# Optimization experiments

Measured on AMD Instinct MI355X. Metric: run time of the kernel, lower is better.

Reference implementation:

```python
import jax, jax.numpy as jnp
import numpy as np

C = 256
DF = 8
CQK = C // DF  # 32


def setup_inputs() -> dict:
    key = jax.random.key(0)
    ks = jax.random.split(key, 7)
    s = 0.02
    x = jax.random.normal(ks[0], (4, C, 64, 64), dtype=jnp.float32)
    Wq = jax.random.normal(ks[1], (CQK, C), dtype=jnp.float32) * s
    bq = jnp.zeros((CQK,), dtype=jnp.float32)
    Wk = jax.random.normal(ks[2], (CQK, C), dtype=jnp.float32) * s
    bk = jnp.zeros((CQK,), dtype=jnp.float32)
    Wv = jax.random.normal(ks[3], (C, C), dtype=jnp.float32) * s
    bv = jnp.zeros((C,), dtype=jnp.float32)
    gamma = jnp.ones((1,), dtype=jnp.float32)  # nonzero so output is nontrivial
    return {"x": x, "Wq": Wq, "bq": bq, "Wk": Wk, "bk": bk, "Wv": Wv, "bv": bv, "gamma": gamma}


def reference(x, Wq, bq, Wk, bk, Wv, bv, gamma):
    B, Cc, H, W = x.shape
    # flatten spatial: [B, N, C] with N = H*W
    xf = x.reshape(B, Cc, H * W).transpose(0, 2, 1)
    # 1x1 convs == per-pixel linear projections
    q = jnp.einsum('bnc,dc->bnd', xf, Wq) + bq        # [B, N, Cqk]
    k = jnp.einsum('bnc,dc->bnd', xf, Wk) + bk        # [B, N, Cqk]
    v = jnp.einsum('bnc,dc->bnd', xf, Wv) + bv        # [B, N, C]
    energy = jnp.einsum('bnd,bmd->bnm', q, k)          # [B, N, N], no scale (as in source)
    attn = jax.nn.softmax(energy, axis=-1)
    out = jnp.einsum('bnm,bmc->bnc', attn, v)          # [B, N, C]
    out = out.transpose(0, 2, 1).reshape(B, Cc, H, W)
    return gamma[0] * out
```

## Files before the change

kernel.cpp:

```cpp
#include <hip/hip_runtime.h>
#include <hip/hip_bf16.h>


typedef __attribute__((ext_vector_type(8))) short s8v;
typedef __attribute__((ext_vector_type(4))) float f4v;

#define NPIX 4096
#define CIN 256
#define DQK 32

#if __has_builtin(__builtin_amdgcn_exp2f)
#define EXP2(x) __builtin_amdgcn_exp2f(x)
#else
#define EXP2(x) exp2f(x)
#endif

#if __has_builtin(__builtin_amdgcn_s_waitcnt)
#define LGKM0_BARRIER() { __builtin_amdgcn_s_waitcnt(0xC07F); __builtin_amdgcn_s_barrier(); }
#else
#define LGKM0_BARRIER() { __asm__ __volatile__("s_waitcnt lgkmcnt(0)\n\ts_barrier" ::: "memory"); }
#endif

static __device__ __forceinline__ unsigned short f2bf(float f) {
    union { float f; unsigned int u; } v; v.f = f;
    unsigned int r = v.u + 0x7FFF + ((v.u >> 16) & 1);
    return (unsigned short)(r >> 16);
}
static __device__ __forceinline__ unsigned int fbits(float f) {
    union { float f; unsigned int u; } v; v.f = f; return v.u;
}

__global__ void wcast_kernel(const float* __restrict__ Wq, const float* __restrict__ bq,
                             const float* __restrict__ Wk, const float* __restrict__ bk,
                             const float* __restrict__ Wv, const float* __restrict__ bv,
                             unsigned short* __restrict__ Wall, float* __restrict__ ball) {
    int row = blockIdx.x;
    int t = threadIdx.x;
    const float* src; const float* bsrc;
    if (row < 32)       { src = Wq + row * 256;        bsrc = bq + row; }
    else if (row < 64)  { src = Wk + (row - 32) * 256; bsrc = bk + (row - 32); }
    else                { src = Wv + (row - 64) * 256; bsrc = bv + (row - 64); }
    Wall[row * 256 + t] = f2bf(src[t]);
    if (t == 0) ball[row] = bsrc[0];
}

__global__ void tcast_kernel(const float* __restrict__ x, unsigned short* __restrict__ xT) {
    __shared__ unsigned short tile[64][65];
    int bidx = blockIdx.x;
    int b    = bidx >> 8;
    int cblk = (bidx >> 6) & 3;
    int nblk = bidx & 63;
    int t = threadIdx.x;
    int c0 = cblk * 64, n0 = nblk * 64;
    const float* xb = x + (size_t)b * CIN * NPIX;
    #pragma unroll
    for (int p = 0; p < 4; p++) {
        int cl = p * 16 + (t >> 4);
        int nl = (t & 15) * 4;
        float4 v = *(const float4*)(xb + (size_t)(c0 + cl) * NPIX + n0 + nl);
        tile[cl][nl + 0] = f2bf(v.x);
        tile[cl][nl + 1] = f2bf(v.y);
        tile[cl][nl + 2] = f2bf(v.z);
        tile[cl][nl + 3] = f2bf(v.w);
    }
    __syncthreads();
    unsigned short* xTb = xT + (size_t)b * NPIX * CIN;
    #pragma unroll
    for (int p = 0; p < 4; p++) {
        int nl = p * 16 + (t >> 4);
        int cl = (t & 15) * 4;
        ushort4 wv;
        wv.x = tile[cl + 0][nl];
        wv.y = tile[cl + 1][nl];
        wv.z = tile[cl + 2][nl];
        wv.w = tile[cl + 3][nl];
        *(ushort4*)(xTb + (size_t)(n0 + nl) * CIN + c0 + cl) = wv;
    }
}

__global__ __launch_bounds__(256)
void proj_kernel(const unsigned short* __restrict__ xT,
                 const unsigned short* __restrict__ Wall,
                 const float* __restrict__ ball,
                 unsigned short* __restrict__ Q,
                 unsigned short* __restrict__ Kp,
                 unsigned short* __restrict__ Vt) {
    int idx  = blockIdx.x;
    int b    = (idx & 7) >> 1;
    int nblk = ((idx >> 3) << 1) | (idx & 1);
    int w    = threadIdx.x >> 6;
    int lane = threadIdx.x & 63;
    int l16 = lane & 15, quad = lane >> 4;
    int n0 = nblk * 64 + w * 16;

    const unsigned short* brow = xT + (size_t)(b * NPIX + n0 + l16) * CIN + quad * 8;
    s8v bfr[8];
    #pragma unroll
    for (int kk = 0; kk < 8; kk++) bfr[kk] = *(const s8v*)(brow + kk * 32);

    #pragma unroll
    for (int p = 0; p < 10; p++) {
        const unsigned short* w0 = Wall + (size_t)(2 * p * 16 + l16) * CIN + quad * 8;
        const unsigned short* w1 = w0 + 16 * CIN;
        f4v a0 = {0.f, 0.f, 0.f, 0.f}, a1 = {0.f, 0.f, 0.f, 0.f};
        if (p < 2) {
            #pragma unroll
            for (int kk = 0; kk < 8; kk++) {
                a0 = __builtin_amdgcn_mfma_f32_16x16x32_bf16(bfr[kk], *(const s8v*)(w0 + kk * 32), a0, 0, 0, 0);
                a1 = __builtin_amdgcn_mfma_f32_16x16x32_bf16(bfr[kk], *(const s8v*)(w1 + kk * 32), a1, 0, 0, 0);
            }
        } else {
            #pragma unroll
            for (int kk = 0; kk < 8; kk++) {
                a0 = __builtin_amdgcn_mfma_f32_16x16x32_bf16(*(const s8v*)(w0 + kk * 32), bfr[kk], a0, 0, 0, 0);
                a1 = __builtin_amdgcn_mfma_f32_16x16x32_bf16(*(const s8v*)(w1 + kk * 32), bfr[kk], a1, 0, 0, 0);
            }
        }
        #pragma unroll
        for (int half = 0; half < 2; half++) {
            int ob = 2 * p + half;
            f4v acc = half ? a1 : a0;
            if (ob < 2) {
                int oc = ob * 16 + l16;
                float bias = ball[oc];
                #pragma unroll
                for (int r = 0; r < 4; r++) {
                    int n = n0 + quad * 4 + r;
                    Q[(size_t)(b * NPIX + n) * DQK + oc] =
                        f2bf((acc[r] + bias) * 1.44269504f);
                }
            } else if (ob < 4) {
                int oc = (ob - 2) * 16 + l16;
                float bias = ball[32 + oc];
                #pragma unroll
                for (int r = 0; r < 4; r++) {
                    int n = n0 + quad * 4 + r;
                    int pn = (n & ~31) | (((n >> 2) & 1) << 4) | (((n >> 3) & 3) << 2) | (n & 3);
                    Kp[(size_t)(b * NPIX + pn) * DQK + oc] = f2bf(acc[r] + bias);
                }
            } else {
                int n = n0 + l16;
                #pragma unroll
                for (int r = 0; r < 4; r++) {
                    int ch = (ob - 4) * 16 + quad * 4 + r;
                    Vt[((size_t)b * CIN + ch) * NPIX + n] = f2bf(acc[r] + ball[64 + ch]);
                }
            }
        }
    }
}

#define ATTN_STEP(S, WB, KC0, KC1, VC, KN0, KN1, VN)                            \
    {                                                                           \
        const int kvn = ((S) + 1) & 63;                                         \
        KN0 = *(const s8v*)(kbase + (size_t)(kvn * 64) * DQK);                  \
        KN1 = *(const s8v*)(kbase + (size_t)(kvn * 64 + 16) * DQK);             \
        _Pragma("unroll")                                                       \
        for (int ct = 0; ct < 4; ct++)                                          \
            VN[ct] = *(const s8v*)(vbase + (size_t)ct * 16 * NPIX + (S) * 64);  \
        const unsigned int* rb = smemw + khw + (1 - (WB)) * 1024;               \
        s8v pa0 = (cj == 0) ? ppv : *(const s8v*)(rb + rdo0);                   \
        s8v pa1 = (cj == 1) ? ppv : *(const s8v*)(rb + rdo1);                   \
        s8v pa2 = (cj == 2) ? ppv : *(const s8v*)(rb + rdo2);                   \
        s8v pa3 = (cj == 3) ? ppv : *(const s8v*)(rb + rdo3);                   \
        f4v s0 = {0.f, 0.f, 0.f, 0.f}, s1 = {0.f, 0.f, 0.f, 0.f};               \
        s0 = __builtin_amdgcn_mfma_f32_16x16x32_bf16(KC0, qf, s0, 0, 0, 0);     \
        s1 = __builtin_amdgcn_mfma_f32_16x16x32_bf16(KC1, qf, s1, 0, 0, 0);     \
        float p00 = EXP2(s0[0]), p01 = EXP2(s0[1]);                             \
        float p02 = EXP2(s0[2]), p03 = EXP2(s0[3]);                             \
        float p10 = EXP2(s1[0]), p11 = EXP2(s1[1]);                             \
        float p12 = EXP2(s1[2]), p13 = EXP2(s1[3]);                             \
        lsum += ((p00 + p01) + (p02 + p03)) + ((p10 + p11) + (p12 + p13));      \
        union { uint4 u; s8v v; } pp;                                           \
        pp.u.x = __builtin_amdgcn_perm(fbits(p01), fbits(p00), 0x07060302);     \
        pp.u.y = __builtin_amdgcn_perm(fbits(p03), fbits(p02), 0x07060302);     \
        pp.u.z = __builtin_amdgcn_perm(fbits(p11), fbits(p10), 0x07060302);     \
        pp.u.w = __builtin_amdgcn_perm(fbits(p13), fbits(p12), 0x07060302);     \
        *(uint4*)(smemw + khw + (WB) * 1024 + wro) = pp.u;                      \
        _Pragma("unroll")                                                       \
        for (int ct = 0; ct < 4; ct++) {                                        \
            O[0][ct] = __builtin_amdgcn_mfma_f32_16x16x32_bf16(VC[ct], pa0, O[0][ct], 0, 0, 0); \
            O[1][ct] = __builtin_amdgcn_mfma_f32_16x16x32_bf16(VC[ct], pa1, O[1][ct], 0, 0, 0); \
            O[2][ct] = __builtin_amdgcn_mfma_f32_16x16x32_bf16(VC[ct], pa2, O[2][ct], 0, 0, 0); \
            O[3][ct] = __builtin_amdgcn_mfma_f32_16x16x32_bf16(VC[ct], pa3, O[3][ct], 0, 0, 0); \
        }                                                                       \
        LGKM0_BARRIER();                                                        \
        ppv = pp.v;                                                             \
    }

__global__ __launch_bounds__(512)
void attn_kernel(const unsigned short* __restrict__ Q,
                 const unsigned short* __restrict__ Kp,
                 const unsigned short* __restrict__ Vt,
                 const float* __restrict__ gamma,
                 float* __restrict__ out) {
    __shared__ __align__(16) char smem[70144];
    unsigned int* smemw = (unsigned int*)smem;

    int idx = blockIdx.x;
    int b      = (idx & 7) >> 1;
    int rowblk = ((idx >> 3) << 1) | (idx & 1);

    int lane = threadIdx.x & 63;
    int w    = threadIdx.x >> 6;
    int l16 = lane & 15, quad = lane >> 4;
    int kh = w >> 2;
    int cj = w & 3;

    const unsigned short* Kb = Kp + (size_t)b * NPIX * DQK;
    const unsigned short* Vb = Vt + (size_t)b * CIN * NPIX;

    int rowbase = rowblk * 64;
    const s8v qf = *(const s8v*)(Q + (size_t)(b * NPIX + rowbase + cj * 16 + l16) * DQK + quad * 8);

    const unsigned short* kbase = Kb + (32 * kh + l16) * DQK + quad * 8;
    const unsigned short* vbase = Vb + (size_t)(cj * 64 + l16) * NPIX + 32 * kh + quad * 8;

    const int khw  = kh * 2048;
    const int wro  = l16 * 64 + (((cj * 4 + quad) ^ (l16 & 7)) << 2);
    const int rdo0 = l16 * 64 + (((0 * 4 + quad) ^ (l16 & 7)) << 2);
    const int rdo1 = l16 * 64 + (((1 * 4 + quad) ^ (l16 & 7)) << 2);
    const int rdo2 = l16 * 64 + (((2 * 4 + quad) ^ (l16 & 7)) << 2);
    const int rdo3 = l16 * 64 + (((3 * 4 + quad) ^ (l16 & 7)) << 2);

    f4v O[4][4];
    #pragma unroll
    for (int rt = 0; rt < 4; rt++)
        #pragma unroll
        for (int ct = 0; ct < 4; ct++) O[rt][ct] = (f4v){0.f, 0.f, 0.f, 0.f};
    float lsum = 0.f;
    s8v ppv;

    s8v Kc0, Kc1, Kn0, Kn1, Vc[4], Vn[4];
    Kc0 = *(const s8v*)(kbase);
    Kc1 = *(const s8v*)(kbase + 16 * DQK);

    {
        Kn0 = *(const s8v*)(kbase + (size_t)64 * DQK);
        Kn1 = *(const s8v*)(kbase + (size_t)80 * DQK);
        #pragma unroll
        for (int ct = 0; ct < 4; ct++)
            Vc[ct] = *(const s8v*)(vbase + (size_t)ct * 16 * NPIX);
        f4v s0 = {0.f, 0.f, 0.f, 0.f}, s1 = {0.f, 0.f, 0.f, 0.f};
        s0 = __builtin_amdgcn_mfma_f32_16x16x32_bf16(Kc0, qf, s0, 0, 0, 0);
        s1 = __builtin_amdgcn_mfma_f32_16x16x32_bf16(Kc1, qf, s1, 0, 0, 0);
        float p00 = EXP2(s0[0]), p01 = EXP2(s0[1]);
        float p02 = EXP2(s0[2]), p03 = EXP2(s0[3]);
        float p10 = EXP2(s1[0]), p11 = EXP2(s1[1]);
        float p12 = EXP2(s1[2]), p13 = EXP2(s1[3]);
        lsum += ((p00 + p01) + (p02 + p03)) + ((p10 + p11) + (p12 + p13));
        union { uint4 u; s8v v; } pp;
        pp.u.x = __builtin_amdgcn_perm(fbits(p01), fbits(p00), 0x07060302);
        pp.u.y = __builtin_amdgcn_perm(fbits(p03), fbits(p02), 0x07060302);
        pp.u.z = __builtin_amdgcn_perm(fbits(p11), fbits(p10), 0x07060302);
        pp.u.w = __builtin_amdgcn_perm(fbits(p13), fbits(p12), 0x07060302);
        *(uint4*)(smemw + khw + 0 * 1024 + wro) = pp.u;
        LGKM0_BARRIER();
        ppv = pp.v;
    }

    for (int p = 0; p < 31; p++) {
        int s1i = 2 * p + 1;
        ATTN_STEP(s1i,     1, Kn0, Kn1, Vc, Kc0, Kc1, Vn);
        ATTN_STEP(s1i + 1, 0, Kc0, Kc1, Vn, Kn0, Kn1, Vc);
    }
    ATTN_STEP(63, 1, Kn0, Kn1, Vc, Kc0, Kc1, Vn);

    {
        const unsigned int* rb = smemw + khw + 1024;
        s8v pa0 = (cj == 0) ? ppv : *(const s8v*)(rb + rdo0);
        s8v pa1 = (cj == 1) ? ppv : *(const s8v*)(rb + rdo1);
        s8v pa2 = (cj == 2) ? ppv : *(const s8v*)(rb + rdo2);
        s8v pa3 = (cj == 3) ? ppv : *(const s8v*)(rb + rdo3);
        #pragma unroll
        for (int ct = 0; ct < 4; ct++) {
            O[0][ct] = __builtin_amdgcn_mfma_f32_16x16x32_bf16(Vn[ct], pa0, O[0][ct], 0, 0, 0);
            O[1][ct] = __builtin_amdgcn_mfma_f32_16x16x32_bf16(Vn[ct], pa1, O[1][ct], 0, 0, 0);
            O[2][ct] = __builtin_amdgcn_mfma_f32_16x16x32_bf16(Vn[ct], pa2, O[2][ct], 0, 0, 0);
            O[3][ct] = __builtin_amdgcn_mfma_f32_16x16x32_bf16(Vn[ct], pa3, O[3][ct], 0, 0, 0);
        }
    }

    lsum += __shfl_xor(lsum, 16);
    lsum += __shfl_xor(lsum, 32);

    __syncthreads();

    float (*ldsO)[64][68] = (float (*)[64][68])smem;
    float* ldsL = (float*)(smem + 69632);

    if (quad == 0) ldsL[kh * 64 + cj * 16 + l16] = lsum;
    if (kh == 1) {
        #pragma unroll
        for (int rt = 0; rt < 4; rt++)
            #pragma unroll
            for (int ct = 0; ct < 4; ct++)
                *(f4v*)&ldsO[cj][lane][(rt * 4 + ct) * 4] = O[rt][ct];
    }
    __syncthreads();

    if (kh == 0) {
        float g = gamma[0];
        float rinv[4];
        #pragma unroll
        for (int rt = 0; rt < 4; rt++)
            rinv[rt] = g / (ldsL[rt * 16 + l16] + ldsL[64 + rt * 16 + l16]);
        #pragma unroll
        for (int rt = 0; rt < 4; rt++) {
            #pragma unroll
            for (int ct = 0; ct < 4; ct++) {
                f4v o2 = *(const f4v*)&ldsO[cj][lane][(rt * 4 + ct) * 4];
                #pragma unroll
                for (int r = 0; r < 4; r++) {
                    int ch = cj * 64 + ct * 16 + quad * 4 + r;
                    out[((size_t)b * CIN + ch) * NPIX + rowbase + rt * 16 + l16] =
                        (O[rt][ct][r] + o2[r]) * rinv[rt];
                }
            }
        }
    }
}

extern "C" void kernel_launch(void* const* d_in, const int* in_sizes, int n_in,
                              void* d_out, int out_size, void* d_ws, size_t ws_size,
                              hipStream_t stream) {
    const float* x     = (const float*)d_in[0];
    const float* Wq    = (const float*)d_in[1];
    const float* bq    = (const float*)d_in[2];
    const float* Wk    = (const float*)d_in[3];
    const float* bk    = (const float*)d_in[4];
    const float* Wv    = (const float*)d_in[5];
    const float* bv    = (const float*)d_in[6];
    const float* gamma = (const float*)d_in[7];
    float* out = (float*)d_out;

    char* p = (char*)d_ws;
    unsigned short* xT   = (unsigned short*)p; p += (size_t)4 * NPIX * CIN * 2;
    unsigned short* Qb   = (unsigned short*)p; p += (size_t)4 * NPIX * DQK * 2;
    unsigned short* Kb   = (unsigned short*)p; p += (size_t)4 * NPIX * DQK * 2;
    unsigned short* Vt   = (unsigned short*)p; p += (size_t)4 * CIN * NPIX * 2;
    unsigned short* Wall = (unsigned short*)p; p += (size_t)320 * 256 * 2;
    float*          ball = (float*)p;          p += (size_t)320 * 4;

    wcast_kernel<<<320, 256, 0, stream>>>(Wq, bq, Wk, bk, Wv, bv, Wall, ball);
    tcast_kernel<<<1024, 256, 0, stream>>>(x, xT);
    proj_kernel<<<256, 256, 0, stream>>>(xT, Wall, ball, Qb, Kb, Vt);
    attn_kernel<<<256, 512, 0, stream>>>(Qb, Kb, Vt, gamma, out);
}
```

Before: 183.4 us.

## Batch four attention steps per LDS barrier with deeper P buffering

Restructures the attention main loop so each wave computes four consecutive QK/softmax sub-steps, writing P tiles into four LDS slots per buffer set, before one barrier. Previously there was a barrier after every step. The change cuts barrier count by four and lets the PV MFMAs of one interval overlap the QK work of the next. In exchange it quadruples per-kh LDS usage for P (khw stride from 2048 to 8192 words), holds four P fragments in registers, and lengthens the V-load pipeline lag, which raises register pressure.

```diff
diff --git a/kernel.cpp b/kernel.cpp
--- a/kernel.cpp
+++ b/kernel.cpp
@@ -150,19 +150,25 @@
     }
 }
 
-#define ATTN_STEP(S, WB, KC0, KC1, VC, KN0, KN1, VN)                            \
+#define SUB_STEP(TB, J, SETW, DOPV, DOVL, KC0, KC1, KN0, KN1, VC, VN, PPV)      \
     {                                                                           \
-        const int kvn = ((S) + 1) & 63;                                         \
+        const int t_ = (TB) + (J);                                              \
+        const int kvn = (t_ + 1) & 63;                                          \
         KN0 = *(const s8v*)(kbase + (size_t)(kvn * 64) * DQK);                  \
         KN1 = *(const s8v*)(kbase + (size_t)(kvn * 64 + 16) * DQK);             \
-        _Pragma("unroll")                                                       \
-        for (int ct = 0; ct < 4; ct++)                                          \
-            VN[ct] = *(const s8v*)(vbase + (size_t)ct * 16 * NPIX + (S) * 64);  \
-        const unsigned int* rb = smemw + khw + (1 - (WB)) * 1024;               \
-        s8v pa0 = (cj == 0) ? ppv : *(const s8v*)(rb + rdo0);                   \
-        s8v pa1 = (cj == 1) ? ppv : *(const s8v*)(rb + rdo1);                   \
-        s8v pa2 = (cj == 2) ? ppv : *(const s8v*)(rb + rdo2);                   \
-        s8v pa3 = (cj == 3) ? ppv : *(const s8v*)(rb + rdo3);                   \
+        if (DOVL) {                                                             \
+            _Pragma("unroll")                                                   \
+            for (int ct = 0; ct < 4; ct++)                                      \
+                VN[ct] = *(const s8v*)(vbase + (size_t)ct * 16 * NPIX + (t_ - 3) * 64); \
+        }                                                                       \
+        s8v pa0, pa1, pa2, pa3;                                                 \
+        if (DOPV) {                                                             \
+            const unsigned int* rb = smemw + khw + ((1 - (SETW)) * 4 + (J)) * 1024; \
+            pa0 = (cj == 0) ? PPV : *(const s8v*)(rb + rdo0);                   \
+            pa1 = (cj == 1) ? PPV : *(const s8v*)(rb + rdo1);                   \
+            pa2 = (cj == 2) ? PPV : *(const s8v*)(rb + rdo2);                   \
+            pa3 = (cj == 3) ? PPV : *(const s8v*)(rb + rdo3);                   \
+        }                                                                       \
         f4v s0 = {0.f, 0.f, 0.f, 0.f}, s1 = {0.f, 0.f, 0.f, 0.f};               \
         s0 = __builtin_amdgcn_mfma_f32_16x16x32_bf16(KC0, qf, s0, 0, 0, 0);     \
         s1 = __builtin_amdgcn_mfma_f32_16x16x32_bf16(KC1, qf, s1, 0, 0, 0);     \
@@ -176,7 +182,38 @@
         pp.u.y = __builtin_amdgcn_perm(fbits(p03), fbits(p02), 0x07060302);     \
         pp.u.z = __builtin_amdgcn_perm(fbits(p11), fbits(p10), 0x07060302);     \
         pp.u.w = __builtin_amdgcn_perm(fbits(p13), fbits(p12), 0x07060302);     \
-        *(uint4*)(smemw + khw + (WB) * 1024 + wro) = pp.u;                      \
+        *(uint4*)(smemw + khw + ((SETW) * 4 + (J)) * 1024 + wro) = pp.u;        \
+        if (DOPV) {                                                             \
+            _Pragma("unroll")                                                   \
+            for (int ct = 0; ct < 4; ct++) {                                    \
+                O[0][ct] = __builtin_amdgcn_mfma_f32_16x16x32_bf16(VC[ct], pa0, O[0][ct], 0, 0, 0); \
+                O[1][ct] = __builtin_amdgcn_mfma_f32_16x16x32_bf16(VC[ct], pa1, O[1][ct], 0, 0, 0); \
+                O[2][ct] = __builtin_amdgcn_mfma_f32_16x16x32_bf16(VC[ct], pa2, O[2][ct], 0, 0, 0); \
+                O[3][ct] = __builtin_amdgcn_mfma_f32_16x16x32_bf16(VC[ct], pa3, O[3][ct], 0, 0, 0); \
+            }                                                                   \
+        }                                                                       \
+        PPV = pp.v;                                                             \
+    }
+
+#define INTERVAL4(TB, SETW)                                                     \
+    SUB_STEP(TB, 0, SETW, 1, 1, Kc0, Kc1, Kn0, Kn1, Vc, Vn, ppv0)               \
+    SUB_STEP(TB, 1, SETW, 1, 1, Kn0, Kn1, Kc0, Kc1, Vn, Vc, ppv1)               \
+    SUB_STEP(TB, 2, SETW, 1, 1, Kc0, Kc1, Kn0, Kn1, Vc, Vn, ppv2)               \
+    SUB_STEP(TB, 3, SETW, 1, 1, Kn0, Kn1, Kc0, Kc1, Vn, Vc, ppv3)               \
+    LGKM0_BARRIER();
+
+#define EPI_STEP(J, VC, VN, PPV, DOVL)                                          \
+    {                                                                           \
+        if (DOVL) {                                                             \
+            _Pragma("unroll")                                                   \
+            for (int ct = 0; ct < 4; ct++)                                      \
+                VN[ct] = *(const s8v*)(vbase + (size_t)ct * 16 * NPIX + (61 + (J)) * 64); \
+        }                                                                       \
+        const unsigned int* rb = smemw + khw + (4 + (J)) * 1024;                \
+        s8v pa0 = (cj == 0) ? PPV : *(const s8v*)(rb + rdo0);                   \
+        s8v pa1 = (cj == 1) ? PPV : *(const s8v*)(rb + rdo1);                   \
+        s8v pa2 = (cj == 2) ? PPV : *(const s8v*)(rb + rdo2);                   \
+        s8v pa3 = (cj == 3) ? PPV : *(const s8v*)(rb + rdo3);                   \
         _Pragma("unroll")                                                       \
         for (int ct = 0; ct < 4; ct++) {                                        \
             O[0][ct] = __builtin_amdgcn_mfma_f32_16x16x32_bf16(VC[ct], pa0, O[0][ct], 0, 0, 0); \
@@ -184,8 +221,6 @@
             O[2][ct] = __builtin_amdgcn_mfma_f32_16x16x32_bf16(VC[ct], pa2, O[2][ct], 0, 0, 0); \
             O[3][ct] = __builtin_amdgcn_mfma_f32_16x16x32_bf16(VC[ct], pa3, O[3][ct], 0, 0, 0); \
         }                                                                       \
-        LGKM0_BARRIER();                                                        \
-        ppv = pp.v;                                                             \
     }
 
 __global__ __launch_bounds__(512)
@@ -216,7 +251,7 @@
     const unsigned short* kbase = Kb + (32 * kh + l16) * DQK + quad * 8;
     const unsigned short* vbase = Vb + (size_t)(cj * 64 + l16) * NPIX + 32 * kh + quad * 8;
 
-    const int khw  = kh * 2048;
+    const int khw  = kh * 8192;
     const int wro  = l16 * 64 + (((cj * 4 + quad) ^ (l16 & 7)) << 2);
     const int rdo0 = l16 * 64 + (((0 * 4 + quad) ^ (l16 & 7)) << 2);
     const int rdo1 = l16 * 64 + (((1 * 4 + quad) ^ (l16 & 7)) << 2);
@@ -229,57 +264,30 @@
         #pragma unroll
         for (int ct = 0; ct < 4; ct++) O[rt][ct] = (f4v){0.f, 0.f, 0.f, 0.f};
     float lsum = 0.f;
-    s8v ppv;
+    s8v ppv0, ppv1, ppv2, ppv3;
 
     s8v Kc0, Kc1, Kn0, Kn1, Vc[4], Vn[4];
     Kc0 = *(const s8v*)(kbase);
     Kc1 = *(const s8v*)(kbase + 16 * DQK);
 
-    {
-        Kn0 = *(const s8v*)(kbase + (size_t)64 * DQK);
-        Kn1 = *(const s8v*)(kbase + (size_t)80 * DQK);
-        #pragma unroll
-        for (int ct = 0; ct < 4; ct++)
-            Vc[ct] = *(const s8v*)(vbase + (size_t)ct * 16 * NPIX);
-        f4v s0 = {0.f, 0.f, 0.f, 0.f}, s1 = {0.f, 0.f, 0.f, 0.f};
-        s0 = __builtin_amdgcn_mfma_f32_16x16x32_bf16(Kc0, qf, s0, 0, 0, 0);
-        s1 = __builtin_amdgcn_mfma_f32_16x16x32_bf16(Kc1, qf, s1, 0, 0, 0);
-        float p00 = EXP2(s0[0]), p01 = EXP2(s0[1]);
-        float p02 = EXP2(s0[2]), p03 = EXP2(s0[3]);
-        float p10 = EXP2(s1[0]), p11 = EXP2(s1[1]);
-        float p12 = EXP2(s1[2]), p13 = EXP2(s1[3]);
-        lsum += ((p00 + p01) + (p02 + p03)) + ((p10 + p11) + (p12 + p13));
-        union { uint4 u; s8v v; } pp;
-        pp.u.x = __builtin_amdgcn_perm(fbits(p01), fbits(p00), 0x07060302);
-        pp.u.y = __builtin_amdgcn_perm(fbits(p03), fbits(p02), 0x07060302);
-        pp.u.z = __builtin_amdgcn_perm(fbits(p11), fbits(p10), 0x07060302);
-        pp.u.w = __builtin_amdgcn_perm(fbits(p13), fbits(p12), 0x07060302);
-        *(uint4*)(smemw + khw + 0 * 1024 + wro) = pp.u;
-        LGKM0_BARRIER();
-        ppv = pp.v;
-    }
-
-    for (int p = 0; p < 31; p++) {
-        int s1i = 2 * p + 1;
-        ATTN_STEP(s1i,     1, Kn0, Kn1, Vc, Kc0, Kc1, Vn);
-        ATTN_STEP(s1i + 1, 0, Kc0, Kc1, Vn, Kn0, Kn1, Vc);
-    }
-    ATTN_STEP(63, 1, Kn0, Kn1, Vc, Kc0, Kc1, Vn);
-
-    {
-        const unsigned int* rb = smemw + khw + 1024;
-        s8v pa0 = (cj == 0) ? ppv : *(const s8v*)(rb + rdo0);
-        s8v pa1 = (cj == 1) ? ppv : *(const s8v*)(rb + rdo1);
-        s8v pa2 = (cj == 2) ? ppv : *(const s8v*)(rb + rdo2);
-        s8v pa3 = (cj == 3) ? ppv : *(const s8v*)(rb + rdo3);
-        #pragma unroll
-        for (int ct = 0; ct < 4; ct++) {
-            O[0][ct] = __builtin_amdgcn_mfma_f32_16x16x32_bf16(Vn[ct], pa0, O[0][ct], 0, 0, 0);
-            O[1][ct] = __builtin_amdgcn_mfma_f32_16x16x32_bf16(Vn[ct], pa1, O[1][ct], 0, 0, 0);
-            O[2][ct] = __builtin_amdgcn_mfma_f32_16x16x32_bf16(Vn[ct], pa2, O[2][ct], 0, 0, 0);
-            O[3][ct] = __builtin_amdgcn_mfma_f32_16x16x32_bf16(Vn[ct], pa3, O[3][ct], 0, 0, 0);
-        }
-    }
+    SUB_STEP(0, 0, 0, 0, 0, Kc0, Kc1, Kn0, Kn1, Vc, Vn, ppv0)
+    SUB_STEP(0, 1, 0, 0, 0, Kn0, Kn1, Kc0, Kc1, Vn, Vc, ppv1)
+    SUB_STEP(0, 2, 0, 0, 0, Kc0, Kc1, Kn0, Kn1, Vc, Vn, ppv2)
+    SUB_STEP(0, 3, 0, 0, 1, Kn0, Kn1, Kc0, Kc1, Vn, Vc, ppv3)
+    LGKM0_BARRIER();
+
+    int tb = 4;
+    for (int p = 0; p < 7; p++) {
+        INTERVAL4(tb, 1)
+        INTERVAL4(tb + 4, 0)
+        tb += 8;
+    }
+    INTERVAL4(60, 1)
+
+    EPI_STEP(0, Vc, Vn, ppv0, 1)
+    EPI_STEP(1, Vn, Vc, ppv1, 1)
+    EPI_STEP(2, Vc, Vn, ppv2, 1)
+    EPI_STEP(3, Vn, Vc, ppv3, 0)
 
     lsum += __shfl_xor(lsum, 16);
     lsum += __shfl_xor(lsum, 32);
```

After: 184.5 us. No clear change (+0.6%).

## Split attention key range across two wave groups with 1024-thread blocks

Applied to the files above, without the earlier changes.

Doubles the attention block to 1024 threads. The key/value sequence is split into two halves handled by separate 8-wave groups, each running 32 steps instead of 64, and the partial outputs and row sums are combined through LDS at the end. The aim is to shorten each block's serial loop and raise the number of waves per CU, since only 256 blocks run on a device with 256 CUs. In exchange it uses about 140KB of dynamic LDS, adds extra reduction barriers, and may raise register pressure under the 1024-thread launch bound. It also relies on dynamic shared memory above the default limit.

```diff
diff --git a/kernel.cpp b/kernel.cpp
--- a/kernel.cpp
+++ b/kernel.cpp
@@ -8,6 +8,7 @@
 #define NPIX 4096
 #define CIN 256
 #define DQK 32
+#define ATTN_LDS 140288
 
 #if __has_builtin(__builtin_amdgcn_exp2f)
 #define EXP2(x) __builtin_amdgcn_exp2f(x)
@@ -152,13 +153,13 @@
 
 #define ATTN_STEP(S, WB, KC0, KC1, VC, KN0, KN1, VN)                            \
     {                                                                           \
-        const int kvn = ((S) + 1) & 63;                                         \
+        const int kvn = ((S) + 1) & 31;                                         \
         KN0 = *(const s8v*)(kbase + (size_t)(kvn * 64) * DQK);                  \
         KN1 = *(const s8v*)(kbase + (size_t)(kvn * 64 + 16) * DQK);             \
         _Pragma("unroll")                                                       \
         for (int ct = 0; ct < 4; ct++)                                          \
             VN[ct] = *(const s8v*)(vbase + (size_t)ct * 16 * NPIX + (S) * 64);  \
-        const unsigned int* rb = smemw + khw + (1 - (WB)) * 1024;               \
+        const unsigned int* rb = smemw + gw + (1 - (WB)) * 1024;                \
         s8v pa0 = (cj == 0) ? ppv : *(const s8v*)(rb + rdo0);                   \
         s8v pa1 = (cj == 1) ? ppv : *(const s8v*)(rb + rdo1);                   \
         s8v pa2 = (cj == 2) ? ppv : *(const s8v*)(rb + rdo2);                   \
@@ -176,7 +177,7 @@
         pp.u.y = __builtin_amdgcn_perm(fbits(p03), fbits(p02), 0x07060302);     \
         pp.u.z = __builtin_amdgcn_perm(fbits(p11), fbits(p10), 0x07060302);     \
         pp.u.w = __builtin_amdgcn_perm(fbits(p13), fbits(p12), 0x07060302);     \
-        *(uint4*)(smemw + khw + (WB) * 1024 + wro) = pp.u;                      \
+        *(uint4*)(smemw + gw + (WB) * 1024 + wro) = pp.u;                       \
         _Pragma("unroll")                                                       \
         for (int ct = 0; ct < 4; ct++) {                                        \
             O[0][ct] = __builtin_amdgcn_mfma_f32_16x16x32_bf16(VC[ct], pa0, O[0][ct], 0, 0, 0); \
@@ -188,13 +189,13 @@
         ppv = pp.v;                                                             \
     }
 
-__global__ __launch_bounds__(512)
+__global__ __launch_bounds__(1024)
 void attn_kernel(const unsigned short* __restrict__ Q,
                  const unsigned short* __restrict__ Kp,
                  const unsigned short* __restrict__ Vt,
                  const float* __restrict__ gamma,
                  float* __restrict__ out) {
-    __shared__ __align__(16) char smem[70144];
+    extern __shared__ __align__(16) char smem[];
     unsigned int* smemw = (unsigned int*)smem;
 
     int idx = blockIdx.x;
@@ -204,8 +205,10 @@
     int lane = threadIdx.x & 63;
     int w    = threadIdx.x >> 6;
     int l16 = lane & 15, quad = lane >> 4;
-    int kh = w >> 2;
-    int cj = w & 3;
+    int khalf = w >> 3;
+    int kh    = (w >> 2) & 1;
+    int cj    = w & 3;
+    int grp   = khalf * 2 + kh;
 
     const unsigned short* Kb = Kp + (size_t)b * NPIX * DQK;
     const unsigned short* Vb = Vt + (size_t)b * CIN * NPIX;
@@ -213,10 +216,10 @@
     int rowbase = rowblk * 64;
     const s8v qf = *(const s8v*)(Q + (size_t)(b * NPIX + rowbase + cj * 16 + l16) * DQK + quad * 8);
 
-    const unsigned short* kbase = Kb + (32 * kh + l16) * DQK + quad * 8;
-    const unsigned short* vbase = Vb + (size_t)(cj * 64 + l16) * NPIX + 32 * kh + quad * 8;
-
-    const int khw  = kh * 2048;
+    const unsigned short* kbase = Kb + (size_t)(khalf * 2048 + 32 * kh + l16) * DQK + quad * 8;
+    const unsigned short* vbase = Vb + (size_t)(cj * 64 + l16) * NPIX + khalf * 2048 + 32 * kh + quad * 8;
+
+    const int gw   = grp * 2048;
     const int wro  = l16 * 64 + (((cj * 4 + quad) ^ (l16 & 7)) << 2);
     const int rdo0 = l16 * 64 + (((0 * 4 + quad) ^ (l16 & 7)) << 2);
     const int rdo1 = l16 * 64 + (((1 * 4 + quad) ^ (l16 & 7)) << 2);
@@ -254,20 +257,20 @@
         pp.u.y = __builtin_amdgcn_perm(fbits(p03), fbits(p02), 0x07060302);
         pp.u.z = __builtin_amdgcn_perm(fbits(p11), fbits(p10), 0x07060302);
         pp.u.w = __builtin_amdgcn_perm(fbits(p13), fbits(p12), 0x07060302);
-        *(uint4*)(smemw + khw + 0 * 1024 + wro) = pp.u;
+        *(uint4*)(smemw + gw + 0 * 1024 + wro) = pp.u;
         LGKM0_BARRIER();
         ppv = pp.v;
     }
 
-    for (int p = 0; p < 31; p++) {
+    for (int p = 0; p < 15; p++) {
         int s1i = 2 * p + 1;
         ATTN_STEP(s1i,     1, Kn0, Kn1, Vc, Kc0, Kc1, Vn);
         ATTN_STEP(s1i + 1, 0, Kc0, Kc1, Vn, Kn0, Kn1, Vc);
     }
-    ATTN_STEP(63, 1, Kn0, Kn1, Vc, Kc0, Kc1, Vn);
+    ATTN_STEP(31, 1, Kn0, Kn1, Vc, Kc0, Kc1, Vn);
 
     {
-        const unsigned int* rb = smemw + khw + 1024;
+        const unsigned int* rb = smemw + gw + 1024;
         s8v pa0 = (cj == 0) ? ppv : *(const s8v*)(rb + rdo0);
         s8v pa1 = (cj == 1) ? ppv : *(const s8v*)(rb + rdo1);
         s8v pa2 = (cj == 2) ? ppv : *(const s8v*)(rb + rdo2);
@@ -286,30 +289,52 @@
 
     __syncthreads();
 
-    float (*ldsO)[64][68] = (float (*)[64][68])smem;
-    float* ldsL = (float*)(smem + 69632);
-
-    if (quad == 0) ldsL[kh * 64 + cj * 16 + l16] = lsum;
+    float (*ldsO)[4][64][68] = (float (*)[4][64][68])smem;
+    float* ldsL = (float*)(smem + 139264);
+
+    if (quad == 0) ldsL[grp * 64 + cj * 16 + l16] = lsum;
     if (kh == 1) {
         #pragma unroll
         for (int rt = 0; rt < 4; rt++)
             #pragma unroll
             for (int ct = 0; ct < 4; ct++)
-                *(f4v*)&ldsO[cj][lane][(rt * 4 + ct) * 4] = O[rt][ct];
+                *(f4v*)&ldsO[khalf][cj][lane][(rt * 4 + ct) * 4] = O[rt][ct];
     }
     __syncthreads();
 
     if (kh == 0) {
+        #pragma unroll
+        for (int rt = 0; rt < 4; rt++)
+            #pragma unroll
+            for (int ct = 0; ct < 4; ct++) {
+                f4v o2 = *(const f4v*)&ldsO[khalf][cj][lane][(rt * 4 + ct) * 4];
+                O[rt][ct][0] += o2[0]; O[rt][ct][1] += o2[1];
+                O[rt][ct][2] += o2[2]; O[rt][ct][3] += o2[3];
+            }
+    }
+    __syncthreads();
+
+    if (kh == 0 && khalf == 1) {
+        #pragma unroll
+        for (int rt = 0; rt < 4; rt++)
+            #pragma unroll
+            for (int ct = 0; ct < 4; ct++)
+                *(f4v*)&ldsO[1][cj][lane][(rt * 4 + ct) * 4] = O[rt][ct];
+    }
+    __syncthreads();
+
+    if (kh == 0 && khalf == 0) {
         float g = gamma[0];
         float rinv[4];
         #pragma unroll
         for (int rt = 0; rt < 4; rt++)
-            rinv[rt] = g / (ldsL[rt * 16 + l16] + ldsL[64 + rt * 16 + l16]);
+            rinv[rt] = g / (ldsL[rt * 16 + l16] + ldsL[64 + rt * 16 + l16] +
+                            ldsL[128 + rt * 16 + l16] + ldsL[192 + rt * 16 + l16]);
         #pragma unroll
         for (int rt = 0; rt < 4; rt++) {
             #pragma unroll
             for (int ct = 0; ct < 4; ct++) {
-                f4v o2 = *(const f4v*)&ldsO[cj][lane][(rt * 4 + ct) * 4];
+                f4v o2 = *(const f4v*)&ldsO[1][cj][lane][(rt * 4 + ct) * 4];
                 #pragma unroll
                 for (int r = 0; r < 4; r++) {
                     int ch = cj * 64 + ct * 16 + quad * 4 + r;
@@ -345,5 +370,5 @@
     wcast_kernel<<<320, 256, 0, stream>>>(Wq, bq, Wk, bk, Wv, bv, Wall, ball);
     tcast_kernel<<<1024, 256, 0, stream>>>(x, xT);
     proj_kernel<<<256, 256, 0, stream>>>(xT, Wall, ball, Qb, Kb, Vt);
-    attn_kernel<<<256, 512, 0, stream>>>(Qb, Kb, Vt, gamma, out);
-}
+    attn_kernel<<<256, 1024, ATTN_LDS, stream>>>(Qb, Kb, Vt, gamma, out);
+}
```

Result: slower. 296.2 us (+61.5%).

## Halve attention row tile to 32 rows and double grid to 512 blocks

Applied to the files above, without the earlier changes.

Each attention block now handles 32 query rows instead of 64, and the grid doubles to 512 blocks. Only the two waves per key-half whose column group matches (isS) compute the QK scores and exp, sharing P through half-size LDS buffers. Each wave keeps half the output accumulators, which should lower register and LDS pressure and fill more CUs on a 256-CU part. In exchange, every K/V tile is streamed twice as many times overall, and the other waves sit idle during the score phase.

```diff
diff --git a/kernel.cpp b/kernel.cpp
--- a/kernel.cpp
+++ b/kernel.cpp
@@ -153,39 +153,39 @@
 #define ATTN_STEP(S, WB, KC0, KC1, VC, KN0, KN1, VN)                            \
     {                                                                           \
         const int kvn = ((S) + 1) & 63;                                         \
-        KN0 = *(const s8v*)(kbase + (size_t)(kvn * 64) * DQK);                  \
-        KN1 = *(const s8v*)(kbase + (size_t)(kvn * 64 + 16) * DQK);             \
+        if (isS) {                                                              \
+            KN0 = *(const s8v*)(kbase + (size_t)(kvn * 64) * DQK);              \
+            KN1 = *(const s8v*)(kbase + (size_t)(kvn * 64 + 16) * DQK);         \
+        }                                                                       \
         _Pragma("unroll")                                                       \
         for (int ct = 0; ct < 4; ct++)                                          \
             VN[ct] = *(const s8v*)(vbase + (size_t)ct * 16 * NPIX + (S) * 64);  \
-        const unsigned int* rb = smemw + khw + (1 - (WB)) * 1024;               \
-        s8v pa0 = (cj == 0) ? ppv : *(const s8v*)(rb + rdo0);                   \
-        s8v pa1 = (cj == 1) ? ppv : *(const s8v*)(rb + rdo1);                   \
-        s8v pa2 = (cj == 2) ? ppv : *(const s8v*)(rb + rdo2);                   \
-        s8v pa3 = (cj == 3) ? ppv : *(const s8v*)(rb + rdo3);                   \
-        f4v s0 = {0.f, 0.f, 0.f, 0.f}, s1 = {0.f, 0.f, 0.f, 0.f};               \
-        s0 = __builtin_amdgcn_mfma_f32_16x16x32_bf16(KC0, qf, s0, 0, 0, 0);     \
-        s1 = __builtin_amdgcn_mfma_f32_16x16x32_bf16(KC1, qf, s1, 0, 0, 0);     \
-        float p00 = EXP2(s0[0]), p01 = EXP2(s0[1]);                             \
-        float p02 = EXP2(s0[2]), p03 = EXP2(s0[3]);                             \
-        float p10 = EXP2(s1[0]), p11 = EXP2(s1[1]);                             \
-        float p12 = EXP2(s1[2]), p13 = EXP2(s1[3]);                             \
-        lsum += ((p00 + p01) + (p02 + p03)) + ((p10 + p11) + (p12 + p13));      \
+        const unsigned int* rb = smemw + khw + (1 - (WB)) * 512;                \
+        s8v pa0 = (isS && srt == 0) ? ppv : *(const s8v*)(rb + rdo0);           \
+        s8v pa1 = (isS && srt == 1) ? ppv : *(const s8v*)(rb + rdo1);           \
         union { uint4 u; s8v v; } pp;                                           \
-        pp.u.x = __builtin_amdgcn_perm(fbits(p01), fbits(p00), 0x07060302);     \
-        pp.u.y = __builtin_amdgcn_perm(fbits(p03), fbits(p02), 0x07060302);     \
-        pp.u.z = __builtin_amdgcn_perm(fbits(p11), fbits(p10), 0x07060302);     \
-        pp.u.w = __builtin_amdgcn_perm(fbits(p13), fbits(p12), 0x07060302);     \
-        *(uint4*)(smemw + khw + (WB) * 1024 + wro) = pp.u;                      \
+        if (isS) {                                                              \
+            f4v s0 = {0.f, 0.f, 0.f, 0.f}, s1 = {0.f, 0.f, 0.f, 0.f};           \
+            s0 = __builtin_amdgcn_mfma_f32_16x16x32_bf16(KC0, qf, s0, 0, 0, 0); \
+            s1 = __builtin_amdgcn_mfma_f32_16x16x32_bf16(KC1, qf, s1, 0, 0, 0); \
+            float p00 = EXP2(s0[0]), p01 = EXP2(s0[1]);                         \
+            float p02 = EXP2(s0[2]), p03 = EXP2(s0[3]);                         \
+            float p10 = EXP2(s1[0]), p11 = EXP2(s1[1]);                         \
+            float p12 = EXP2(s1[2]), p13 = EXP2(s1[3]);                         \
+            lsum += ((p00 + p01) + (p02 + p03)) + ((p10 + p11) + (p12 + p13));  \
+            pp.u.x = __builtin_amdgcn_perm(fbits(p01), fbits(p00), 0x07060302); \
+            pp.u.y = __builtin_amdgcn_perm(fbits(p03), fbits(p02), 0x07060302); \
+            pp.u.z = __builtin_amdgcn_perm(fbits(p11), fbits(p10), 0x07060302); \
+            pp.u.w = __builtin_amdgcn_perm(fbits(p13), fbits(p12), 0x07060302); \
+            *(uint4*)(smemw + khw + (WB) * 512 + wro) = pp.u;                   \
+        }                                                                       \
         _Pragma("unroll")                                                       \
         for (int ct = 0; ct < 4; ct++) {                                        \
             O[0][ct] = __builtin_amdgcn_mfma_f32_16x16x32_bf16(VC[ct], pa0, O[0][ct], 0, 0, 0); \
             O[1][ct] = __builtin_amdgcn_mfma_f32_16x16x32_bf16(VC[ct], pa1, O[1][ct], 0, 0, 0); \
-            O[2][ct] = __builtin_amdgcn_mfma_f32_16x16x32_bf16(VC[ct], pa2, O[2][ct], 0, 0, 0); \
-            O[3][ct] = __builtin_amdgcn_mfma_f32_16x16x32_bf16(VC[ct], pa3, O[3][ct], 0, 0, 0); \
         }                                                                       \
         LGKM0_BARRIER();                                                        \
-        ppv = pp.v;                                                             \
+        if (isS) ppv = pp.v;                                                    \
     }
 
 __global__ __launch_bounds__(512)
@@ -194,7 +194,7 @@
                  const unsigned short* __restrict__ Vt,
                  const float* __restrict__ gamma,
                  float* __restrict__ out) {
-    __shared__ __align__(16) char smem[70144];
+    __shared__ __align__(16) char smem[37120];
     unsigned int* smemw = (unsigned int*)smem;
 
     int idx = blockIdx.x;
@@ -206,57 +206,63 @@
     int l16 = lane & 15, quad = lane >> 4;
     int kh = w >> 2;
     int cj = w & 3;
+    int srt = cj & 1;
+    int isS = ((cj >> 1) == kh);
 
     const unsigned short* Kb = Kp + (size_t)b * NPIX * DQK;
     const unsigned short* Vb = Vt + (size_t)b * CIN * NPIX;
 
-    int rowbase = rowblk * 64;
-    const s8v qf = *(const s8v*)(Q + (size_t)(b * NPIX + rowbase + cj * 16 + l16) * DQK + quad * 8);
+    int rowbase = rowblk * 32;
+    const s8v qf = *(const s8v*)(Q + (size_t)(b * NPIX + rowbase + srt * 16 + l16) * DQK + quad * 8);
 
     const unsigned short* kbase = Kb + (32 * kh + l16) * DQK + quad * 8;
     const unsigned short* vbase = Vb + (size_t)(cj * 64 + l16) * NPIX + 32 * kh + quad * 8;
 
-    const int khw  = kh * 2048;
-    const int wro  = l16 * 64 + (((cj * 4 + quad) ^ (l16 & 7)) << 2);
-    const int rdo0 = l16 * 64 + (((0 * 4 + quad) ^ (l16 & 7)) << 2);
-    const int rdo1 = l16 * 64 + (((1 * 4 + quad) ^ (l16 & 7)) << 2);
-    const int rdo2 = l16 * 64 + (((2 * 4 + quad) ^ (l16 & 7)) << 2);
-    const int rdo3 = l16 * 64 + (((3 * 4 + quad) ^ (l16 & 7)) << 2);
-
-    f4v O[4][4];
-    #pragma unroll
-    for (int rt = 0; rt < 4; rt++)
+    const int khw  = kh * 1024;
+    const int wro  = l16 * 32 + (((srt * 4 + quad) ^ (l16 & 7)) << 2);
+    const int rdo0 = l16 * 32 + (((0 * 4 + quad) ^ (l16 & 7)) << 2);
+    const int rdo1 = l16 * 32 + (((1 * 4 + quad) ^ (l16 & 7)) << 2);
+
+    f4v O[2][4];
+    #pragma unroll
+    for (int rt = 0; rt < 2; rt++)
         #pragma unroll
         for (int ct = 0; ct < 4; ct++) O[rt][ct] = (f4v){0.f, 0.f, 0.f, 0.f};
     float lsum = 0.f;
     s8v ppv;
 
     s8v Kc0, Kc1, Kn0, Kn1, Vc[4], Vn[4];
-    Kc0 = *(const s8v*)(kbase);
-    Kc1 = *(const s8v*)(kbase + 16 * DQK);
+    if (isS) {
+        Kc0 = *(const s8v*)(kbase);
+        Kc1 = *(const s8v*)(kbase + 16 * DQK);
+    }
 
     {
-        Kn0 = *(const s8v*)(kbase + (size_t)64 * DQK);
-        Kn1 = *(const s8v*)(kbase + (size_t)80 * DQK);
+        if (isS) {
+            Kn0 = *(const s8v*)(kbase + (size_t)64 * DQK);
+            Kn1 = *(const s8v*)(kbase + (size_t)80 * DQK);
+        }
         #pragma unroll
         for (int ct = 0; ct < 4; ct++)
             Vc[ct] = *(const s8v*)(vbase + (size_t)ct * 16 * NPIX);
-        f4v s0 = {0.f, 0.f, 0.f, 0.f}, s1 = {0.f, 0.f, 0.f, 0.f};
-        s0 = __builtin_amdgcn_mfma_f32_16x16x32_bf16(Kc0, qf, s0, 0, 0, 0);
-        s1 = __builtin_amdgcn_mfma_f32_16x16x32_bf16(Kc1, qf, s1, 0, 0, 0);
-        float p00 = EXP2(s0[0]), p01 = EXP2(s0[1]);
-        float p02 = EXP2(s0[2]), p03 = EXP2(s0[3]);
-        float p10 = EXP2(s1[0]), p11 = EXP2(s1[1]);
-        float p12 = EXP2(s1[2]), p13 = EXP2(s1[3]);
-        lsum += ((p00 + p01) + (p02 + p03)) + ((p10 + p11) + (p12 + p13));
-        union { uint4 u; s8v v; } pp;
-        pp.u.x = __builtin_amdgcn_perm(fbits(p01), fbits(p00), 0x07060302);
-        pp.u.y = __builtin_amdgcn_perm(fbits(p03), fbits(p02), 0x07060302);
-        pp.u.z = __builtin_amdgcn_perm(fbits(p11), fbits(p10), 0x07060302);
-        pp.u.w = __builtin_amdgcn_perm(fbits(p13), fbits(p12), 0x07060302);
-        *(uint4*)(smemw + khw + 0 * 1024 + wro) = pp.u;
+        if (isS) {
+            f4v s0 = {0.f, 0.f, 0.f, 0.f}, s1 = {0.f, 0.f, 0.f, 0.f};
+            s0 = __builtin_amdgcn_mfma_f32_16x16x32_bf16(Kc0, qf, s0, 0, 0, 0);
+            s1 = __builtin_amdgcn_mfma_f32_16x16x32_bf16(Kc1, qf, s1, 0, 0, 0);
+            float p00 = EXP2(s0[0]), p01 = EXP2(s0[1]);
+            float p02 = EXP2(s0[2]), p03 = EXP2(s0[3]);
+            float p10 = EXP2(s1[0]), p11 = EXP2(s1[1]);
+            float p12 = EXP2(s1[2]), p13 = EXP2(s1[3]);
+            lsum += ((p00 + p01) + (p02 + p03)) + ((p10 + p11) + (p12 + p13));
+            union { uint4 u; s8v v; } pp;
+            pp.u.x = __builtin_amdgcn_perm(fbits(p01), fbits(p00), 0x07060302);
+            pp.u.y = __builtin_amdgcn_perm(fbits(p03), fbits(p02), 0x07060302);
+            pp.u.z = __builtin_amdgcn_perm(fbits(p11), fbits(p10), 0x07060302);
+            pp.u.w = __builtin_amdgcn_perm(fbits(p13), fbits(p12), 0x07060302);
+            *(uint4*)(smemw + khw + 0 * 512 + wro) = pp.u;
+            ppv = pp.v;
+        }
         LGKM0_BARRIER();
-        ppv = pp.v;
     }
 
     for (int p = 0; p < 31; p++) {
@@ -267,17 +273,13 @@
     ATTN_STEP(63, 1, Kn0, Kn1, Vc, Kc0, Kc1, Vn);
 
     {
-        const unsigned int* rb = smemw + khw + 1024;
-        s8v pa0 = (cj == 0) ? ppv : *(const s8v*)(rb + rdo0);
-        s8v pa1 = (cj == 1) ? ppv : *(const s8v*)(rb + rdo1);
-        s8v pa2 = (cj == 2) ? ppv : *(const s8v*)(rb + rdo2);
-        s8v pa3 = (cj == 3) ? ppv : *(const s8v*)(rb + rdo3);
+        const unsigned int* rb = smemw + khw + 512;
+        s8v pa0 = (isS && srt == 0) ? ppv : *(const s8v*)(rb + rdo0);
+        s8v pa1 = (isS && srt == 1) ? ppv : *(const s8v*)(rb + rdo1);
         #pragma unroll
         for (int ct = 0; ct < 4; ct++) {
             O[0][ct] = __builtin_amdgcn_mfma_f32_16x16x32_bf16(Vn[ct], pa0, O[0][ct], 0, 0, 0);
             O[1][ct] = __builtin_amdgcn_mfma_f32_16x16x32_bf16(Vn[ct], pa1, O[1][ct], 0, 0, 0);
-            O[2][ct] = __builtin_amdgcn_mfma_f32_16x16x32_bf16(Vn[ct], pa2, O[2][ct], 0, 0, 0);
-            O[3][ct] = __builtin_amdgcn_mfma_f32_16x16x32_bf16(Vn[ct], pa3, O[3][ct], 0, 0, 0);
         }
     }
 
@@ -286,13 +288,13 @@
 
     __syncthreads();
 
-    float (*ldsO)[64][68] = (float (*)[64][68])smem;
-    float* ldsL = (float*)(smem + 69632);
-
-    if (quad == 0) ldsL[kh * 64 + cj * 16 + l16] = lsum;
+    float (*ldsO)[64][36] = (float (*)[64][36])smem;
+    float* ldsL = (float*)(smem + 36864);
+
+    if (isS && quad == 0) ldsL[kh * 32 + srt * 16 + l16] = lsum;
     if (kh == 1) {
         #pragma unroll
-        for (int rt = 0; rt < 4; rt++)
+        for (int rt = 0; rt < 2; rt++)
             #pragma unroll
             for (int ct = 0; ct < 4; ct++)
                 *(f4v*)&ldsO[cj][lane][(rt * 4 + ct) * 4] = O[rt][ct];
@@ -301,12 +303,12 @@
 
     if (kh == 0) {
         float g = gamma[0];
-        float rinv[4];
-        #pragma unroll
-        for (int rt = 0; rt < 4; rt++)
-            rinv[rt] = g / (ldsL[rt * 16 + l16] + ldsL[64 + rt * 16 + l16]);
-        #pragma unroll
-        for (int rt = 0; rt < 4; rt++) {
+        float rinv[2];
+        #pragma unroll
+        for (int rt = 0; rt < 2; rt++)
+            rinv[rt] = g / (ldsL[rt * 16 + l16] + ldsL[32 + rt * 16 + l16]);
+        #pragma unroll
+        for (int rt = 0; rt < 2; rt++) {
             #pragma unroll
             for (int ct = 0; ct < 4; ct++) {
                 f4v o2 = *(const f4v*)&ldsO[cj][lane][(rt * 4 + ct) * 4];
@@ -345,5 +347,5 @@
     wcast_kernel<<<320, 256, 0, stream>>>(Wq, bq, Wk, bk, Wv, bv, Wall, ball);
     tcast_kernel<<<1024, 256, 0, stream>>>(x, xT);
     proj_kernel<<<256, 256, 0, stream>>>(xT, Wall, ball, Qb, Kb, Vt);
-    attn_kernel<<<256, 512, 0, stream>>>(Qb, Kb, Vt, gamma, out);
-}
+    attn_kernel<<<512, 512, 0, stream>>>(Qb, Kb, Vt, gamma, out);
+}
```

Result: slower. 239.0 us (+30.3%).
